# Performance work log

Hardware: AMD Instinct MI355X
Metric: run time of the kernel (lower is better)

## Reference

```python
import jax, jax.numpy as jnp
import numpy as np

HEADS = 8
DIM_HEAD = 64
BN_EPS = 1e-5

def setup_inputs() -> dict:
    key = jax.random.key(0)
    ks = jax.random.split(key, 6)
    B, N, D = 8, 1024, 512
    inner = HEADS * DIM_HEAD  # 512
    return {
        "x": jax.random.normal(ks[0], (B, N, D), dtype=jnp.float32),
        "w_qkv": jax.random.normal(ks[1], (D, 3 * inner), dtype=jnp.float32) * (D ** -0.5),
        "conv_w": jax.random.normal(ks[2], (HEADS, HEADS), dtype=jnp.float32) * (HEADS ** -0.5),
        "conv_b": jax.random.normal(ks[3], (HEADS,), dtype=jnp.float32) * 0.02,
        "bn_gamma": jnp.ones((HEADS,), dtype=jnp.float32),
        "bn_beta": jnp.zeros((HEADS,), dtype=jnp.float32),
        "w_out": jax.random.normal(ks[4], (inner, D), dtype=jnp.float32) * (inner ** -0.5),
        "b_out": jnp.zeros((D,), dtype=jnp.float32),
    }

def reference(x, w_qkv, conv_w, conv_b, bn_gamma, bn_beta, w_out, b_out):
    B, N, D = x.shape
    H, dh = HEADS, DIM_HEAD
    scale = dh ** -0.5
    qkv = x @ w_qkv  # [B, N, 3*H*dh]
    q, k, v = jnp.split(qkv, 3, axis=-1)
    # b n (h d) -> b h n d
    q = q.reshape(B, N, H, dh).transpose(0, 2, 1, 3)
    k = k.reshape(B, N, H, dh).transpose(0, 2, 1, 3)
    v = v.reshape(B, N, H, dh).transpose(0, 2, 1, 3)
    attn = jnp.einsum('bhnd,bhmd->bhnm', q, k) * scale
    attn = jax.nn.softmax(attn, axis=-1)
    # 1x1 conv across heads (channels = heads)
    attn = jnp.einsum('gh,bhnm->bgnm', conv_w, attn) + conv_b[None, :, None, None]
    # BatchNorm2d in training mode: batch stats over (B, N, N) per head, biased variance
    mean = attn.mean(axis=(0, 2, 3), keepdims=True)
    var = attn.var(axis=(0, 2, 3), keepdims=True)
    attn = (attn - mean) * jax.lax.rsqrt(var + BN_EPS)
    attn = attn * bn_gamma[None, :, None, None] + bn_beta[None, :, None, None]
    # reatten_scale = 1.0 (transform_scale=False)
    out = jnp.einsum('bhnm,bhmd->bhnd', attn, v)
    out = out.transpose(0, 2, 1, 3).reshape(B, N, H * dh)  # b h n d -> b n (h d)
    return out @ w_out + b_out
```

## Files before the change

kernel.cpp:

```cpp
#include <hip/hip_runtime.h>
#include <math.h>


#define Bz 8
#define Nn 1024
#define Dd 512
#define Hh 8
#define DH 64
#define INNER 512
#define QW 1536
#define SCALE 0.125f
#define BN_EPS 1e-5f

typedef _Float16 __f16;
typedef __f16 f16x8 __attribute__((ext_vector_type(8)));
typedef __f16 f16x2 __attribute__((ext_vector_type(2)));
typedef __fp16 fp16x2 __attribute__((ext_vector_type(2)));
typedef float f32x4 __attribute__((ext_vector_type(4)));

#define MFMA16(a, b, c) __builtin_amdgcn_mfma_f32_16x16x32_f16((a), (b), (c), 0, 0, 0)

__device__ __forceinline__ unsigned short f2h(float f) {
  union { __f16 h; unsigned short s; } v;
  v.h = (__f16)f;
  return v.s;
}
__device__ __forceinline__ float h2f(unsigned short s) {
  union { unsigned short s; __f16 h; } v;
  v.s = s;
  return (float)v.h;
}

#define WB_XB 0u
#define WB_QKV 8388608u
#define WB_O1 0u
#define WB_VT 33554432u
#define WB_SG 41943040u
#define WB_O1BF WB_SG
#define WB_WQT 176160768u
#define WB_WOT 177733632u
#define WB_RSUM 178257920u
#define WB_VSUM 178520064u
#define WB_STATS 178536448u
#define WB_AC 178536512u

__global__ __launch_bounds__(256) void k_xbf(const float* __restrict__ X,
                                             unsigned short* __restrict__ XB) {
  const size_t i = ((size_t)blockIdx.x * 256 + threadIdx.x) * 8;
  float4 f0 = *(const float4*)(X + i);
  float4 f1 = *(const float4*)(X + i + 4);
  unsigned short o[8] = {f2h(f0.x), f2h(f0.y), f2h(f0.z), f2h(f0.w),
                         f2h(f1.x), f2h(f1.y), f2h(f1.z), f2h(f1.w)};
  *(uint4*)(XB + i) = *(uint4*)o;
}

__global__ __launch_bounds__(256) void k_transpose(const float* __restrict__ src,
                                                   unsigned short* __restrict__ dst,
                                                   int R, int C) {
  __shared__ float tile[32][33];
  const int tc = blockIdx.x * 32, tr = blockIdx.y * 32;
  const int lx = threadIdx.x & 31, ly = threadIdx.x >> 5;
#pragma unroll
  for (int i = 0; i < 32; i += 8)
    tile[ly + i][lx] = src[(size_t)(tr + ly + i) * C + tc + lx];
  __syncthreads();
#pragma unroll
  for (int i = 0; i < 32; i += 8)
    dst[(size_t)(tc + ly + i) * R + tr + lx] = f2h(tile[lx][ly + i]);
}

__global__ __launch_bounds__(256) void k_qkv(const unsigned short* __restrict__ XB,
                                             const unsigned short* __restrict__ WQT,
                                             unsigned short* __restrict__ qkv,
                                             unsigned short* __restrict__ vT) {
  extern __shared__ char smem[];
  unsigned short(*sA)[40] = (unsigned short(*)[40])smem;
  unsigned short(*sB)[40] = (unsigned short(*)[40])(smem + 128 * 40 * 2);
  unsigned short* sEp = (unsigned short*)smem;
  const int t = threadIdx.x;
  const int col0 = blockIdx.x * 128;
  const int row0 = blockIdx.y * 128;
  const bool isqk = (col0 < 2 * INNER);
  const int l = t & 63, w = t >> 6;
  const int wm = (w & 1) * 64, wn = (w >> 1) * 64;
  const int lm = l & 15, lq = l >> 4;
  const int srow = t >> 1, skc = (t & 1) * 16;
  f32x4 acc[4][4] = {};
  for (int k0 = 0; k0 < Dd; k0 += 32) {
    {
      const unsigned short* src = XB + (size_t)(row0 + srow) * Dd + k0 + skc;
      *(uint4*)&sA[srow][skc] = *(const uint4*)src;
      *(uint4*)&sA[srow][skc + 8] = *(const uint4*)(src + 8);
    }
    {
      const unsigned short* srcB = WQT + (size_t)(col0 + srow) * Dd + k0 + skc;
      *(uint4*)&sB[srow][skc] = *(const uint4*)srcB;
      *(uint4*)&sB[srow][skc + 8] = *(const uint4*)(srcB + 8);
    }
    __syncthreads();
    f16x8 af[4], bfr[4];
#pragma unroll
    for (int i = 0; i < 4; i++) af[i] = *(const f16x8*)&sA[wm + 16 * i + lm][lq * 8];
#pragma unroll
    for (int j = 0; j < 4; j++) bfr[j] = *(const f16x8*)&sB[wn + 16 * j + lm][lq * 8];
    if (isqk) {
#pragma unroll
      for (int i = 0; i < 4; i++)
#pragma unroll
        for (int j = 0; j < 4; j++) acc[i][j] = MFMA16(bfr[i], af[j], acc[i][j]);
    } else {
#pragma unroll
      for (int i = 0; i < 4; i++)
#pragma unroll
        for (int j = 0; j < 4; j++) acc[i][j] = MFMA16(af[i], bfr[j], acc[i][j]);
    }
    __syncthreads();
  }
  if (isqk) {
#pragma unroll
    for (int jc = 0; jc < 4; jc++)
#pragma unroll
      for (int ir = 0; ir < 4; ir++) {
        unsigned short us[4];
#pragma unroll
        for (int r = 0; r < 4; r++) us[r] = f2h(acc[jc][ir][r]);
        *(uint2*)&sEp[(wm + 16 * ir + lm) * 136 + wn + 16 * jc + 4 * lq] = *(uint2*)us;
      }
    __syncthreads();
    const int row = t >> 1, half = t & 1;
    const unsigned short* src = &sEp[row * 136 + half * 64];
    unsigned short* dst = qkv + (size_t)(row0 + row) * QW + col0 + half * 64;
#pragma unroll
    for (int c = 0; c < 8; c++) *(uint4*)(dst + c * 8) = *(const uint4*)(src + c * 8);
  } else {
#pragma unroll
    for (int ir = 0; ir < 4; ir++)
#pragma unroll
      for (int jc = 0; jc < 4; jc++) {
        unsigned short us[4];
#pragma unroll
        for (int r = 0; r < 4; r++) us[r] = f2h(acc[ir][jc][r]);
        *(uint2*)&sEp[(wn + 16 * jc + lm) * 136 + wm + 16 * ir + 4 * lq] = *(uint2*)us;
      }
    __syncthreads();
    const int row = t >> 1, half = t & 1;
    const int gd = col0 - 2 * INNER + row;
    const int bq = row0 >> 10, mseq0 = row0 & 1023;
    const unsigned short* src = &sEp[row * 136 + half * 64];
    unsigned short* dst =
        vT + (((size_t)(bq * Hh + (gd >> 6)) * DH + (gd & 63)) << 10) + mseq0 + half * 64;
#pragma unroll
    for (int c = 0; c < 8; c++) *(uint4*)(dst + c * 8) = *(const uint4*)(src + c * 8);
  }
}

__global__ __launch_bounds__(256) void k_vsum(const unsigned short* __restrict__ vT,
                                              float* __restrict__ vsum) {
  const int bg = blockIdx.x;
  const int d = threadIdx.x >> 2, qq = threadIdx.x & 3;
  __shared__ float red[64][4];
  const unsigned short* p = vT + ((size_t)bg * DH + d) * Nn + qq * 256;
  float s = 0.f;
  for (int m = 0; m < 256; m += 4) {
    uint2 rr = *(const uint2*)(p + m);
    s += h2f((unsigned short)(rr.x & 0xffff)) + h2f((unsigned short)(rr.x >> 16)) +
         h2f((unsigned short)(rr.y & 0xffff)) + h2f((unsigned short)(rr.y >> 16));
  }
  red[d][qq] = s;
  __syncthreads();
  if (threadIdx.x < 64)
    vsum[(size_t)bg * DH + threadIdx.x] =
        red[threadIdx.x][0] + red[threadIdx.x][1] + red[threadIdx.x][2] + red[threadIdx.x][3];
}

__global__ __launch_bounds__(512, 2) void k_sgen(const unsigned short* __restrict__ qkv,
                                                 unsigned short* __restrict__ Sg,
                                                 float* __restrict__ rsum) {
  __shared__ unsigned short sK[8 * 32 * 72];
  __shared__ unsigned short sT[32 * 264];
  const int b = blockIdx.x;
  const int n0 = blockIdx.y * 32;
  const int mh = blockIdx.z;
  const int t = threadIdx.x;
  const int w = t >> 6, l = t & 63;
  const int lm = l & 15, lq = l >> 4;
  f16x8 qf[2][2];
#pragma unroll
  for (int i = 0; i < 2; i++) {
    const unsigned short* qp =
        qkv + (size_t)(b * Nn + n0 + 16 * i + lm) * QW + w * DH + lq * 8;
    qf[i][0] = *(const f16x8*)qp;
    qf[i][1] = *(const f16x8*)(qp + 32);
  }
  float psum[2] = {0.f, 0.f};
  for (int it = 0; it < 16; it++) {
    const int m0 = mh * 512 + it * 32;
    {
#pragma unroll
      for (int s = 0; s < 4; s++) {
        const int c = t + s * 512;
        const int hh = c >> 8, mm = (c >> 3) & 31, qq = c & 7;
        *(uint4*)&sK[(hh * 32 + mm) * 72 + qq * 8] = *(const uint4*)(
            qkv + (size_t)(b * Nn + m0 + mm) * QW + INNER + hh * DH + qq * 8);
      }
    }
    __syncthreads();
    f32x4 lac[2][2] = {};
#pragma unroll
    for (int jm = 0; jm < 2; jm++) {
      f16x8 ka0 = *(const f16x8*)&sK[(w * 32 + 16 * jm + lm) * 72 + lq * 8];
      f16x8 ka1 = *(const f16x8*)&sK[(w * 32 + 16 * jm + lm) * 72 + 32 + lq * 8];
#pragma unroll
      for (int i = 0; i < 2; i++) {
        lac[i][jm] = MFMA16(ka0, qf[i][0], lac[i][jm]);
        lac[i][jm] = MFMA16(ka1, qf[i][1], lac[i][jm]);
      }
    }
#pragma unroll
    for (int i = 0; i < 2; i++)
#pragma unroll
      for (int jm = 0; jm < 2; jm++)
#pragma unroll
        for (int r = 0; r < 4; r++) {
          float e = __expf(lac[i][jm][r] * SCALE);
          psum[i] += e;
          sT[(16 * i + lm) * 264 + (16 * jm + 4 * lq + r) * 8 + w] = f2h(e);
        }
    __syncthreads();
    {
      const int row = t >> 4, ck = t & 15;
      unsigned short* dst =
          Sg + (((size_t)(b * Nn + n0 + row) << 10) + m0) * 8 + ck * 16;
      const unsigned short* src = &sT[row * 264 + ck * 16];
      *(uint4*)dst = *(const uint4*)src;
      *(uint4*)(dst + 8) = *(const uint4*)(src + 8);
    }
  }
#pragma unroll
  for (int i = 0; i < 2; i++) {
    psum[i] += __shfl_xor(psum[i], 16);
    psum[i] += __shfl_xor(psum[i], 32);
  }
  if (lq == 0) {
    atomicAdd(&rsum[(size_t)(b * Hh + w) * Nn + n0 + lm], psum[0]);
    atomicAdd(&rsum[(size_t)(b * Hh + w) * Nn + n0 + 16 + lm], psum[1]);
  }
}

__global__ __launch_bounds__(512, 2) void k_mixsv(const unsigned short* __restrict__ Sg,
                                                  const unsigned short* __restrict__ vT,
                                                  const float* __restrict__ rsum,
                                                  const float* __restrict__ conv_w,
                                                  float* __restrict__ O1,
                                                  float* __restrict__ stats) {
  __shared__ unsigned short sU[2][8][16][68];
  __shared__ float sRed[8][8];
  const int b = blockIdx.x;
  const int n0 = blockIdx.y * 16;
  const int t = threadIdx.x;
  const int w = t >> 6, l = t & 63;
  const int lm = l & 15, lq = l >> 4;
  const int mxn = t >> 5, mxm = (t & 31) * 2;
  float cw[64];
#pragma unroll
  for (int i = 0; i < 64; i++) cw[i] = conv_w[i];
  f16x2 rvh2[4];
#pragma unroll
  for (int hp = 0; hp < 4; hp++) {
    float r0 = 1.0f / rsum[(size_t)(b * Hh + 2 * hp) * Nn + n0 + mxn];
    float r1 = 1.0f / rsum[(size_t)(b * Hh + 2 * hp + 1) * Nn + n0 + mxn];
    f16x2 rr;
    rr[0] = (__f16)r0;
    rr[1] = (__f16)r1;
    rvh2[hp] = rr;
  }
  const unsigned short* sNp = Sg + ((size_t)(b * Nn + n0 + mxn) << 13);
  f32x4 oacc[4] = {};
  float su2[8] = {};
  uint4 c0, c1;
  {
    const unsigned short* p = sNp + (mxm << 3);
    c0 = *(const uint4*)p;
    c1 = *(const uint4*)(p + 8);
  }
  int p = 0;
  for (int it = 0; it < 16; it++) {
    uint4 nx0, nx1;
    if (it < 15) {
      const unsigned short* pp = sNp + ((size_t)((it + 1) * 64 + mxm) << 3);
      nx0 = *(const uint4*)pp;
      nx1 = *(const uint4*)(pp + 8);
    }
    {
      const f16x2* pe2 = (const f16x2*)&c0;
      const f16x2* po2 = (const f16x2*)&c1;
      f16x2 eh[4], oh[4];
#pragma unroll
      for (int hp = 0; hp < 4; hp++) {
        eh[hp] = pe2[hp] * rvh2[hp];
        oh[hp] = po2[hp] * rvh2[hp];
      }
#pragma unroll
      for (int g = 0; g < 8; g++) {
        float u0 = 0.f, u1 = 0.f;
#pragma unroll
        for (int hp = 0; hp < 4; hp++) {
          u0 = fmaf((float)eh[hp][0], cw[g * 8 + 2 * hp], u0);
          u0 = fmaf((float)eh[hp][1], cw[g * 8 + 2 * hp + 1], u0);
          u1 = fmaf((float)oh[hp][0], cw[g * 8 + 2 * hp], u1);
          u1 = fmaf((float)oh[hp][1], cw[g * 8 + 2 * hp + 1], u1);
        }
        su2[g] = fmaf(u0, u0, fmaf(u1, u1, su2[g]));
        fp16x2 pk = __builtin_amdgcn_cvt_pkrtz(u0, u1);
        *(unsigned*)&sU[p][g][mxn][mxm] = *(unsigned*)&pk;
      }
    }
    f16x8 va[4], vb[4];
#pragma unroll
    for (int j = 0; j < 4; j++) {
      const unsigned short* vp =
          vT + (((size_t)(b * Hh + w) * DH + 16 * j + lm) << 10) + it * 64 + lq * 8;
      va[j] = *(const f16x8*)vp;
      vb[j] = *(const f16x8*)(vp + 32);
    }
    __syncthreads();
    {
      f16x8 uf0 = *(const f16x8*)&sU[p][w][lm][lq * 8];
      f16x8 uf1 = *(const f16x8*)&sU[p][w][lm][32 + lq * 8];
#pragma unroll
      for (int j = 0; j < 4; j++) {
        oacc[j] = MFMA16(uf0, va[j], oacc[j]);
        oacc[j] = MFMA16(uf1, vb[j], oacc[j]);
      }
    }
    if (it < 15) {
      c0 = nx0;
      c1 = nx1;
    }
    p ^= 1;
  }
#pragma unroll
  for (int j = 0; j < 4; j++)
#pragma unroll
    for (int r = 0; r < 4; r++)
      O1[((size_t)(b * Hh + w) * Nn + n0 + lq * 4 + r) * DH + 16 * j + lm] = oacc[j][r];
#pragma unroll
  for (int g = 0; g < 8; g++) {
    float q = su2[g];
    for (int off = 32; off; off >>= 1) q += __shfl_down(q, off);
    if (l == 0) sRed[w][g] = q;
  }
  __syncthreads();
  if (t < 8) {
    float s = 0.f;
#pragma unroll
    for (int ww = 0; ww < 8; ww++) s += sRed[ww][t];
    atomicAdd(&stats[8 + t], s);
  }
}

__global__ void k_alpha(const float* __restrict__ stats, const float* __restrict__ conv_w,
                        const float* __restrict__ bn_gamma,
                        const float* __restrict__ bn_beta, float* __restrict__ ac) {
  const int g = threadIdx.x;
  if (g < 8) {
    const float cnt = (float)Bz * (float)Nn * (float)Nn;
    float sc = 0.f;
#pragma unroll
    for (int h = 0; h < 8; h++) sc += conv_w[g * 8 + h];
    float Eu = sc * (1.0f / (float)Nn);
    float Eu2 = stats[8 + g] / cnt;
    float inv = rsqrtf(Eu2 - Eu * Eu + BN_EPS);
    float alpha = bn_gamma[g] * inv;
    ac[g] = alpha;
    ac[8 + g] = bn_beta[g] - Eu * alpha;
  }
}

__global__ __launch_bounds__(256) void k_o1aff(const float* __restrict__ O1,
                                               const float* __restrict__ vsum,
                                               const float* __restrict__ ac,
                                               unsigned short* __restrict__ O1BF) {
  const size_t i4 = ((size_t)blockIdx.x * 256 + threadIdx.x) * 4;
  const int bg = (int)(i4 >> 16);
  const int g = bg & 7;
  const int d = (int)(i4 & 63);
  float4 a = *(const float4*)(O1 + i4);
  float4 v = *(const float4*)(vsum + (size_t)bg * DH + d);
  const float al = ac[g], cc = ac[8 + g];
  unsigned short o[4] = {f2h(al * a.x + cc * v.x), f2h(al * a.y + cc * v.y),
                         f2h(al * a.z + cc * v.z), f2h(al * a.w + cc * v.w)};
  *(uint2*)(O1BF + i4) = *(uint2*)o;
}

__global__ __launch_bounds__(256) void k_out(const unsigned short* __restrict__ O1BF,
                                             const unsigned short* __restrict__ WOT,
                                             const float* __restrict__ bout,
                                             float* __restrict__ out) {
  __shared__ unsigned short sA[128][40];
  __shared__ unsigned short sB[128][40];
  const int t = threadIdx.x;
  const int col0 = blockIdx.x * 128, row0 = blockIdx.y * 128;
  const int l = t & 63, w = t >> 6;
  const int wm = (w & 1) * 64, wn = (w >> 1) * 64;
  const int lm = l & 15, lq = l >> 4;
  const int srow = t >> 1, skc = (t & 1) * 16;
  const int b = row0 >> 10;
  const int nn = (row0 + srow) & 1023;
  f32x4 acc[4][4] = {};
  for (int k0 = 0; k0 < INNER; k0 += 32) {
    {
      const int k = k0 + skc;
      const int g = k >> 6, dd = k & 63;
      const unsigned short* src = O1BF + ((size_t)(b * Hh + g) * Nn + nn) * DH + dd;
      *(uint4*)&sA[srow][skc] = *(const uint4*)src;
      *(uint4*)&sA[srow][skc + 8] = *(const uint4*)(src + 8);
    }
    {
      const unsigned short* srcB = WOT + (size_t)(col0 + srow) * INNER + k0 + skc;
      *(uint4*)&sB[srow][skc] = *(const uint4*)srcB;
      *(uint4*)&sB[srow][skc + 8] = *(const uint4*)(srcB + 8);
    }
    __syncthreads();
    f16x8 af[4], bfr[4];
#pragma unroll
    for (int i = 0; i < 4; i++) af[i] = *(const f16x8*)&sA[wm + 16 * i + lm][lq * 8];
#pragma unroll
    for (int j = 0; j < 4; j++) bfr[j] = *(const f16x8*)&sB[wn + 16 * j + lm][lq * 8];
#pragma unroll
    for (int i = 0; i < 4; i++)
#pragma unroll
      for (int j = 0; j < 4; j++) acc[i][j] = MFMA16(af[i], bfr[j], acc[i][j]);
    __syncthreads();
  }
#pragma unroll
  for (int j = 0; j < 4; j++) {
    const int col = col0 + wn + 16 * j + lm;
    const float bo = bout[col];
#pragma unroll
    for (int i = 0; i < 4; i++) {
      const int rbase = row0 + wm + 16 * i + lq * 4;
#pragma unroll
      for (int r = 0; r < 4; r++) out[(size_t)(rbase + r) * Dd + col] = acc[i][j][r] + bo;
    }
  }
}

extern "C" void kernel_launch(void* const* d_in, const int* in_sizes, int n_in,
                              void* d_out, int out_size, void* d_ws, size_t ws_size,
                              hipStream_t stream) {
  const float* x = (const float*)d_in[0];
  const float* w_qkv = (const float*)d_in[1];
  const float* conv_w = (const float*)d_in[2];
  const float* bn_gamma = (const float*)d_in[4];
  const float* bn_beta = (const float*)d_in[5];
  const float* w_out = (const float*)d_in[6];
  const float* b_out = (const float*)d_in[7];
  char* ws = (char*)d_ws;
  unsigned short* XB = (unsigned short*)(ws + WB_XB);
  unsigned short* QKV = (unsigned short*)(ws + WB_QKV);
  unsigned short* VT = (unsigned short*)(ws + WB_VT);
  unsigned short* SG = (unsigned short*)(ws + WB_SG);
  unsigned short* WQT = (unsigned short*)(ws + WB_WQT);
  unsigned short* WOT = (unsigned short*)(ws + WB_WOT);
  float* O1 = (float*)(ws + WB_O1);
  unsigned short* O1BF = (unsigned short*)(ws + WB_O1BF);
  float* RSUM = (float*)(ws + WB_RSUM);
  float* VSUM = (float*)(ws + WB_VSUM);
  float* STATS = (float*)(ws + WB_STATS);
  float* AC = (float*)(ws + WB_AC);

  hipMemsetAsync(STATS, 0, 64, stream);
  hipMemsetAsync(RSUM, 0, 262144, stream);
  k_xbf<<<2048, 256, 0, stream>>>(x, XB);
  k_transpose<<<dim3(48, 16), 256, 0, stream>>>(w_qkv, WQT, 512, 1536);
  k_transpose<<<dim3(16, 16), 256, 0, stream>>>(w_out, WOT, 512, 512);
  k_qkv<<<dim3(12, 64), 256, 34816, stream>>>(XB, WQT, QKV, VT);
  k_vsum<<<64, 256, 0, stream>>>(VT, VSUM);
  k_sgen<<<dim3(8, 32, 2), 512, 0, stream>>>(QKV, SG, RSUM);
  k_mixsv<<<dim3(8, 64), 512, 0, stream>>>(SG, VT, RSUM, conv_w, O1, STATS);
  k_alpha<<<1, 64, 0, stream>>>(STATS, conv_w, bn_gamma, bn_beta, AC);
  k_o1aff<<<4096, 256, 0, stream>>>(O1, VSUM, AC, O1BF);
  k_out<<<dim3(4, 64), 256, 0, stream>>>(O1BF, WOT, b_out, (float*)d_out);
}
```

Measured before the change: 273.4 us.

## Fuse score generation into mix kernel, recomputing QK^T instead of storing scores

Removes the separate score-generation kernel that wrote fp16 exp scores (B*N*N*H) to global memory and the row-sum atomics. The fused kernel computes QK^T twice per tile: a first pass for the softmax row sums, then a second pass that normalizes, mixes heads through the 1x1 conv, and multiplies by V. This avoids the large score write and read-back, and the rsum memset, at the cost of doubling the QK MFMA and exp work. The fused kernel also reads K straight from global memory without LDS staging.

```diff
diff --git a/kernel.cpp b/kernel.cpp
--- a/kernel.cpp
+++ b/kernel.cpp
@@ -33,13 +33,11 @@
 
 #define WB_XB 0u
 #define WB_QKV 8388608u
-#define WB_O1 0u
 #define WB_VT 33554432u
-#define WB_SG 41943040u
-#define WB_O1BF WB_SG
+#define WB_O1 41943040u
+#define WB_O1BF 58720256u
 #define WB_WQT 176160768u
 #define WB_WOT 177733632u
-#define WB_RSUM 178257920u
 #define WB_VSUM 178520064u
 #define WB_STATS 178536448u
 #define WB_AC 178536512u
@@ -173,87 +171,13 @@
         red[threadIdx.x][0] + red[threadIdx.x][1] + red[threadIdx.x][2] + red[threadIdx.x][3];
 }
 
-__global__ __launch_bounds__(512, 2) void k_sgen(const unsigned short* __restrict__ qkv,
-                                                 unsigned short* __restrict__ Sg,
-                                                 float* __restrict__ rsum) {
-  __shared__ unsigned short sK[8 * 32 * 72];
-  __shared__ unsigned short sT[32 * 264];
-  const int b = blockIdx.x;
-  const int n0 = blockIdx.y * 32;
-  const int mh = blockIdx.z;
-  const int t = threadIdx.x;
-  const int w = t >> 6, l = t & 63;
-  const int lm = l & 15, lq = l >> 4;
-  f16x8 qf[2][2];
-#pragma unroll
-  for (int i = 0; i < 2; i++) {
-    const unsigned short* qp =
-        qkv + (size_t)(b * Nn + n0 + 16 * i + lm) * QW + w * DH + lq * 8;
-    qf[i][0] = *(const f16x8*)qp;
-    qf[i][1] = *(const f16x8*)(qp + 32);
-  }
-  float psum[2] = {0.f, 0.f};
-  for (int it = 0; it < 16; it++) {
-    const int m0 = mh * 512 + it * 32;
-    {
-#pragma unroll
-      for (int s = 0; s < 4; s++) {
-        const int c = t + s * 512;
-        const int hh = c >> 8, mm = (c >> 3) & 31, qq = c & 7;
-        *(uint4*)&sK[(hh * 32 + mm) * 72 + qq * 8] = *(const uint4*)(
-            qkv + (size_t)(b * Nn + m0 + mm) * QW + INNER + hh * DH + qq * 8);
-      }
-    }
-    __syncthreads();
-    f32x4 lac[2][2] = {};
-#pragma unroll
-    for (int jm = 0; jm < 2; jm++) {
-      f16x8 ka0 = *(const f16x8*)&sK[(w * 32 + 16 * jm + lm) * 72 + lq * 8];
-      f16x8 ka1 = *(const f16x8*)&sK[(w * 32 + 16 * jm + lm) * 72 + 32 + lq * 8];
-#pragma unroll
-      for (int i = 0; i < 2; i++) {
-        lac[i][jm] = MFMA16(ka0, qf[i][0], lac[i][jm]);
-        lac[i][jm] = MFMA16(ka1, qf[i][1], lac[i][jm]);
-      }
-    }
-#pragma unroll
-    for (int i = 0; i < 2; i++)
-#pragma unroll
-      for (int jm = 0; jm < 2; jm++)
-#pragma unroll
-        for (int r = 0; r < 4; r++) {
-          float e = __expf(lac[i][jm][r] * SCALE);
-          psum[i] += e;
-          sT[(16 * i + lm) * 264 + (16 * jm + 4 * lq + r) * 8 + w] = f2h(e);
-        }
-    __syncthreads();
-    {
-      const int row = t >> 4, ck = t & 15;
-      unsigned short* dst =
-          Sg + (((size_t)(b * Nn + n0 + row) << 10) + m0) * 8 + ck * 16;
-      const unsigned short* src = &sT[row * 264 + ck * 16];
-      *(uint4*)dst = *(const uint4*)src;
-      *(uint4*)(dst + 8) = *(const uint4*)(src + 8);
-    }
-  }
-#pragma unroll
-  for (int i = 0; i < 2; i++) {
-    psum[i] += __shfl_xor(psum[i], 16);
-    psum[i] += __shfl_xor(psum[i], 32);
-  }
-  if (lq == 0) {
-    atomicAdd(&rsum[(size_t)(b * Hh + w) * Nn + n0 + lm], psum[0]);
-    atomicAdd(&rsum[(size_t)(b * Hh + w) * Nn + n0 + 16 + lm], psum[1]);
-  }
-}
-
-__global__ __launch_bounds__(512, 2) void k_mixsv(const unsigned short* __restrict__ Sg,
-                                                  const unsigned short* __restrict__ vT,
-                                                  const float* __restrict__ rsum,
-                                                  const float* __restrict__ conv_w,
-                                                  float* __restrict__ O1,
-                                                  float* __restrict__ stats) {
-  __shared__ unsigned short sU[2][8][16][68];
+__global__ __launch_bounds__(512, 2) void k_fmix(const unsigned short* __restrict__ qkv,
+                                                 const unsigned short* __restrict__ vT,
+                                                 const float* __restrict__ conv_w,
+                                                 float* __restrict__ O1,
+                                                 float* __restrict__ stats) {
+  __shared__ __align__(16) unsigned short sT[2][16][520];
+  __shared__ __align__(16) unsigned short sU[8][16][68];
   __shared__ float sRed[8][8];
   const int b = blockIdx.x;
   const int n0 = blockIdx.y * 16;
@@ -264,78 +188,84 @@
   float cw[64];
 #pragma unroll
   for (int i = 0; i < 64; i++) cw[i] = conv_w[i];
-  f16x2 rvh2[4];
-#pragma unroll
-  for (int hp = 0; hp < 4; hp++) {
-    float r0 = 1.0f / rsum[(size_t)(b * Hh + 2 * hp) * Nn + n0 + mxn];
-    float r1 = 1.0f / rsum[(size_t)(b * Hh + 2 * hp + 1) * Nn + n0 + mxn];
-    f16x2 rr;
-    rr[0] = (__f16)r0;
-    rr[1] = (__f16)r1;
-    rvh2[hp] = rr;
-  }
-  const unsigned short* sNp = Sg + ((size_t)(b * Nn + n0 + mxn) << 13);
+  const unsigned short* qp = qkv + (size_t)(b * Nn + n0 + lm) * QW + w * DH + lq * 8;
+  const f16x8 qf0 = *(const f16x8*)qp;
+  const f16x8 qf1 = *(const f16x8*)(qp + 32);
+  const unsigned short* kbase = qkv + (size_t)b * Nn * QW + INNER + w * DH + lq * 8;
+  float psum = 0.f;
+  for (int it = 0; it < 16; it++) {
+    const int m0 = it * 64;
+#pragma unroll
+    for (int jm = 0; jm < 4; jm++) {
+      const unsigned short* kp = kbase + (size_t)(m0 + 16 * jm + lm) * QW;
+      f16x8 ka0 = *(const f16x8*)kp;
+      f16x8 ka1 = *(const f16x8*)(kp + 32);
+      f32x4 lac = {};
+      lac = MFMA16(ka0, qf0, lac);
+      lac = MFMA16(ka1, qf1, lac);
+#pragma unroll
+      for (int r = 0; r < 4; r++) psum += __expf(lac[r] * SCALE);
+    }
+  }
+  psum += __shfl_xor(psum, 16);
+  psum += __shfl_xor(psum, 32);
+  const float rv = 1.0f / psum;
   f32x4 oacc[4] = {};
   float su2[8] = {};
-  uint4 c0, c1;
-  {
-    const unsigned short* p = sNp + (mxm << 3);
-    c0 = *(const uint4*)p;
-    c1 = *(const uint4*)(p + 8);
-  }
   int p = 0;
   for (int it = 0; it < 16; it++) {
-    uint4 nx0, nx1;
-    if (it < 15) {
-      const unsigned short* pp = sNp + ((size_t)((it + 1) * 64 + mxm) << 3);
-      nx0 = *(const uint4*)pp;
-      nx1 = *(const uint4*)(pp + 8);
-    }
-    {
+    const int m0 = it * 64;
+    {
+#pragma unroll
+      for (int jm = 0; jm < 4; jm++) {
+        const unsigned short* kp = kbase + (size_t)(m0 + 16 * jm + lm) * QW;
+        f16x8 ka0 = *(const f16x8*)kp;
+        f16x8 ka1 = *(const f16x8*)(kp + 32);
+        f32x4 lac = {};
+        lac = MFMA16(ka0, qf0, lac);
+        lac = MFMA16(ka1, qf1, lac);
+#pragma unroll
+        for (int r = 0; r < 4; r++) {
+          float e = __expf(lac[r] * SCALE) * rv;
+          sT[p][lm][(16 * jm + 4 * lq + r) * 8 + w] = f2h(e);
+        }
+      }
+    }
+    __syncthreads();
+    {
+      const unsigned short* srcT = &sT[p][mxn][mxm * 8];
+      uint4 c0 = *(const uint4*)srcT;
+      uint4 c1 = *(const uint4*)(srcT + 8);
       const f16x2* pe2 = (const f16x2*)&c0;
       const f16x2* po2 = (const f16x2*)&c1;
-      f16x2 eh[4], oh[4];
-#pragma unroll
-      for (int hp = 0; hp < 4; hp++) {
-        eh[hp] = pe2[hp] * rvh2[hp];
-        oh[hp] = po2[hp] * rvh2[hp];
-      }
 #pragma unroll
       for (int g = 0; g < 8; g++) {
         float u0 = 0.f, u1 = 0.f;
 #pragma unroll
         for (int hp = 0; hp < 4; hp++) {
-          u0 = fmaf((float)eh[hp][0], cw[g * 8 + 2 * hp], u0);
-          u0 = fmaf((float)eh[hp][1], cw[g * 8 + 2 * hp + 1], u0);
-          u1 = fmaf((float)oh[hp][0], cw[g * 8 + 2 * hp], u1);
-          u1 = fmaf((float)oh[hp][1], cw[g * 8 + 2 * hp + 1], u1);
+          u0 = fmaf((float)pe2[hp][0], cw[g * 8 + 2 * hp], u0);
+          u0 = fmaf((float)pe2[hp][1], cw[g * 8 + 2 * hp + 1], u0);
+          u1 = fmaf((float)po2[hp][0], cw[g * 8 + 2 * hp], u1);
+          u1 = fmaf((float)po2[hp][1], cw[g * 8 + 2 * hp + 1], u1);
         }
         su2[g] = fmaf(u0, u0, fmaf(u1, u1, su2[g]));
         fp16x2 pk = __builtin_amdgcn_cvt_pkrtz(u0, u1);
-        *(unsigned*)&sU[p][g][mxn][mxm] = *(unsigned*)&pk;
+        *(unsigned*)&sU[g][mxn][mxm] = *(unsigned*)&pk;
       }
     }
-    f16x8 va[4], vb[4];
-#pragma unroll
-    for (int j = 0; j < 4; j++) {
-      const unsigned short* vp =
-          vT + (((size_t)(b * Hh + w) * DH + 16 * j + lm) << 10) + it * 64 + lq * 8;
-      va[j] = *(const f16x8*)vp;
-      vb[j] = *(const f16x8*)(vp + 32);
-    }
-    __syncthreads();
-    {
-      f16x8 uf0 = *(const f16x8*)&sU[p][w][lm][lq * 8];
-      f16x8 uf1 = *(const f16x8*)&sU[p][w][lm][32 + lq * 8];
+    __syncthreads();
+    {
+      f16x8 uf0 = *(const f16x8*)&sU[w][lm][lq * 8];
+      f16x8 uf1 = *(const f16x8*)&sU[w][lm][32 + lq * 8];
+      const unsigned short* vpb =
+          vT + (((size_t)(b * Hh + w) * DH + lm) << 10) + m0 + lq * 8;
 #pragma unroll
       for (int j = 0; j < 4; j++) {
-        oacc[j] = MFMA16(uf0, va[j], oacc[j]);
-        oacc[j] = MFMA16(uf1, vb[j], oacc[j]);
+        f16x8 va = *(const f16x8*)(vpb + (j << 14));
+        f16x8 vb = *(const f16x8*)(vpb + (j << 14) + 32);
+        oacc[j] = MFMA16(uf0, va, oacc[j]);
+        oacc[j] = MFMA16(uf1, vb, oacc[j]);
       }
-    }
-    if (it < 15) {
-      c0 = nx0;
-      c1 = nx1;
     }
     p ^= 1;
   }
@@ -460,25 +390,21 @@
   unsigned short* XB = (unsigned short*)(ws + WB_XB);
   unsigned short* QKV = (unsigned short*)(ws + WB_QKV);
   unsigned short* VT = (unsigned short*)(ws + WB_VT);
-  unsigned short* SG = (unsigned short*)(ws + WB_SG);
   unsigned short* WQT = (unsigned short*)(ws + WB_WQT);
   unsigned short* WOT = (unsigned short*)(ws + WB_WOT);
   float* O1 = (float*)(ws + WB_O1);
   unsigned short* O1BF = (unsigned short*)(ws + WB_O1BF);
-  float* RSUM = (float*)(ws + WB_RSUM);
   float* VSUM = (float*)(ws + WB_VSUM);
   float* STATS = (float*)(ws + WB_STATS);
   float* AC = (float*)(ws + WB_AC);
 
   hipMemsetAsync(STATS, 0, 64, stream);
-  hipMemsetAsync(RSUM, 0, 262144, stream);
   k_xbf<<<2048, 256, 0, stream>>>(x, XB);
   k_transpose<<<dim3(48, 16), 256, 0, stream>>>(w_qkv, WQT, 512, 1536);
   k_transpose<<<dim3(16, 16), 256, 0, stream>>>(w_out, WOT, 512, 512);
   k_qkv<<<dim3(12, 64), 256, 34816, stream>>>(XB, WQT, QKV, VT);
   k_vsum<<<64, 256, 0, stream>>>(VT, VSUM);
-  k_sgen<<<dim3(8, 32, 2), 512, 0, stream>>>(QKV, SG, RSUM);
-  k_mixsv<<<dim3(8, 64), 512, 0, stream>>>(SG, VT, RSUM, conv_w, O1, STATS);
+  k_fmix<<<dim3(8, 64), 512, 0, stream>>>(QKV, VT, conv_w, O1, STATS);
   k_alpha<<<1, 64, 0, stream>>>(STATS, conv_w, bn_gamma, bn_beta, AC);
   k_o1aff<<<4096, 256, 0, stream>>>(O1, VSUM, AC, O1BF);
   k_out<<<dim3(4, 64), 256, 0, stream>>>(O1BF, WOT, b_out, (float*)d_out);
```

Measured after the change: 344.6 us. 26.1% more time.
